# Optimization experiments

Measured on AMD Instinct MI355X. Metric: run time of the kernel, lower is better.

The kernel has to match this reference:

```python
import jax, jax.numpy as jnp
import numpy as np

NUM_NODES = 20000
NUM_EDGES = 65536
WIDTH = 64
EDGE_FEAT = 6
HIDDEN = 128


def setup_inputs() -> dict:
    key = jax.random.key(0)
    ks = jax.random.split(key, 6)
    x = jax.random.normal(ks[0], (NUM_NODES, WIDTH), dtype=jnp.float32)
    edge_attr = jax.random.normal(ks[1], (NUM_EDGES, EDGE_FEAT), dtype=jnp.float32)
    # weight-generating MLP params (the `nn` callable), fan-in scaled
    W1 = jax.random.normal(ks[2], (EDGE_FEAT, HIDDEN), dtype=jnp.float32) / np.sqrt(EDGE_FEAT)
    b1 = jnp.zeros((HIDDEN,), dtype=jnp.float32)
    W2 = jax.random.normal(ks[3], (HIDDEN, WIDTH * WIDTH), dtype=jnp.float32) / np.sqrt(HIDDEN)
    b2 = jnp.zeros((WIDTH * WIDTH,), dtype=jnp.float32)
    senders = jax.random.randint(ks[4], (NUM_EDGES,), 0, NUM_NODES)
    receivers = jax.random.randint(ks[5], (NUM_EDGES,), 0, NUM_NODES)
    return {"x": x, "edge_attr": edge_attr, "W1": W1, "b1": b1,
            "W2": W2, "b2": b2, "senders": senders, "receivers": receivers}


def reference(x, edge_attr, W1, b1, W2, b2, senders, receivers):
    n_segs, width = x.shape
    # nn(edge_attr): (E, width*width) edge-conditioned weights
    h = jax.nn.relu(edge_attr @ W1 + b1)
    weight = (h @ W2 + b2).reshape(-1, width, width)  # (E, w, w)
    # gather sender features, per-edge (1,w) @ (w,w) matmul -> (E, w)
    msgs = jnp.einsum('ew,ewv->ev', x[senders], weight)
    # scatter-sum messages into receiver nodes (aggr == 'sum')
    return jax.ops.segment_sum(msgs, receivers, num_segments=n_segs)
```

## Files before the change

kernel.cpp:

```cpp
#include <hip/hip_runtime.h>
#include <stdint.h>

typedef _Float16 f16;
typedef f16 f16x8 __attribute__((ext_vector_type(8)));
typedef float f32x4 __attribute__((ext_vector_type(4)));

#define NUM_NODES 20000
#define NUM_EDGES 65536
#define WIDTH 64
#define EDGE_FEAT 6
#define HIDDEN 128
#define BM 64
#define PADCH 132
#define XPAD 72

#define XH_HALFS (NUM_NODES * WIDTH)
#define XCONV_BLKS 625
#define W2G_HALFS (PADCH * 4096)
#define OUT_FLOATS (NUM_NODES * WIDTH)
#define ZBLKS 313

__device__ __forceinline__ void gload_lds16(const f16* g, f16* l) {
  __builtin_amdgcn_global_load_lds(
      (const __attribute__((address_space(1))) unsigned int*)g,
      (__attribute__((address_space(3))) unsigned int*)l, 16, 0, 0);
}

__global__ __launch_bounds__(256) void prep_kernel(
    const float* __restrict__ x, const float* __restrict__ W2,
    const float* __restrict__ b2, f16* __restrict__ ws_h,
    float* __restrict__ out)
{
  f16* x_h = ws_h;
  f16* W2g = ws_h + XH_HALFS;
  const int blk = blockIdx.x, tid = threadIdx.x;

  if (blk < PADCH) {
    const int ki = blk;
    if (ki > HIDDEN) {
      f16x8 z;
      #pragma unroll
      for (int u = 0; u < 8; ++u) z[u] = (f16)0.f;
      *(f16x8*)&W2g[(size_t)ki * 4096 + tid * 16] = z;
      *(f16x8*)&W2g[(size_t)ki * 4096 + tid * 16 + 8] = z;
      return;
    }
    __shared__ float row[4096];
    const float* srcrow;
    if (ki < HIDDEN) {
      const float4* src = (const float4*)(W2 + (size_t)ki * 4096);
      #pragma unroll
      for (int i = 0; i < 4; ++i) {
        float4 v = src[tid + 256 * i];
        *(float4*)&row[(tid + 256 * i) * 4] = v;
      }
      __syncthreads();
      srcrow = row;
    } else {
      srcrow = b2;
    }
    const int obase = tid * 16;
    f16x8 outv0, outv1;
    #pragma unroll
    for (int u = 0; u < 8; ++u) {
      int o = obase + u;
      int n = o >> 6, pg = (o >> 3) & 7, j = o & 7;
      int k = (pg ^ (n & 7)) * 8 + j;
      outv0[u] = (f16)srcrow[k * 64 + n];
    }
    #pragma unroll
    for (int u = 0; u < 8; ++u) {
      int o = obase + 8 + u;
      int n = o >> 6, pg = (o >> 3) & 7, j = o & 7;
      int k = (pg ^ (n & 7)) * 8 + j;
      outv1[u] = (f16)srcrow[k * 64 + n];
    }
    *(f16x8*)&W2g[(size_t)ki * 4096 + obase] = outv0;
    *(f16x8*)&W2g[(size_t)ki * 4096 + obase + 8] = outv1;
  } else if (blk < PADCH + XCONV_BLKS) {
    int idx = (blk - PADCH) * 2048 + tid * 8;
    if (idx + 8 <= XH_HALFS) {
      float4 a = *(const float4*)(x + idx);
      float4 b = *(const float4*)(x + idx + 4);
      f16x8 hv;
      hv[0] = (f16)a.x; hv[1] = (f16)a.y; hv[2] = (f16)a.z; hv[3] = (f16)a.w;
      hv[4] = (f16)b.x; hv[5] = (f16)b.y; hv[6] = (f16)b.z; hv[7] = (f16)b.w;
      *(f16x8*)&x_h[idx] = hv;
    }
  } else {
    int base = (blk - PADCH - XCONV_BLKS) * 4096 + tid * 16;
    float4 z = {0.f, 0.f, 0.f, 0.f};
    #pragma unroll
    for (int i = 0; i < 4; ++i) {
      int idx = base + i * 4;
      if (idx + 4 <= OUT_FLOATS) *(float4*)(out + idx) = z;
    }
  }
}

__global__ __launch_bounds__(256, 4) void nnconv_kernel(
    const float* __restrict__ ea, const float* __restrict__ W1,
    const float* __restrict__ b1, const int* __restrict__ senders,
    const int* __restrict__ receivers, const f16* __restrict__ ws_h,
    float* __restrict__ out)
{
  const f16* x_h = ws_h;
  const f16* W2g = ws_h + XH_HALFS;
  __shared__ __align__(16) f16 xt[BM][XPAD];
  __shared__ __align__(16) f16 Bb[2][4096];

  const int tid = threadIdx.x;
  const int lane = tid & 63, wid = tid >> 6;
  const int quad = lane >> 4, l15 = lane & 15;
  const int mhalf = wid >> 1, nhalf = wid & 1;
  const int e0 = blockIdx.x * BM;
  const int mbase = mhalf * 32;

#define STAGE(CI, SP)                                                         \
  {                                                                           \
    _Pragma("unroll") for (int i_ = 0; i_ < 2; ++i_) {                        \
      int slice_ = wid + 4 * i_;                                              \
      gload_lds16(W2g + (size_t)(CI) * 4096 + slice_ * 512 + (lane << 3),     \
                  &Bb[SP][slice_ * 512]);                                     \
    }                                                                         \
  }
  STAGE(0, 0);

  {
    int r = tid >> 2, q = tid & 3;
    int s = senders[e0 + r];
    const uint4* src = (const uint4*)(x_h + (size_t)s * WIDTH + q * 16);
    uint4* dst = (uint4*)&xt[r][q * 16];
    dst[0] = src[0];
    dst[1] = src[1];
  }

  float ear[2][6];
  #pragma unroll
  for (int t = 0; t < 2; ++t) {
    const float* p = ea + (size_t)(e0 + mbase + t * 16 + l15) * EDGE_FEAT;
    #pragma unroll
    for (int f = 0; f < 6; ++f) ear[t][f] = p[f];
  }

  int boff[2][2];
  #pragma unroll
  for (int kc = 0; kc < 2; ++kc)
    #pragma unroll
    for (int nt = 0; nt < 2; ++nt) {
      int n = nhalf * 32 + nt * 16 + l15;
      int g = kc * 4 + quad;
      boff[kc][nt] = n * 64 + (g ^ (n & 7)) * 8;
    }

#define HCOMP(KI, HV)                                                         \
  {                                                                           \
    float b1c_ = b1[(KI)];                                                    \
    float w1c_[6];                                                            \
    _Pragma("unroll") for (int f = 0; f < 6; ++f)                             \
      w1c_[f] = W1[f * HIDDEN + (KI)];                                        \
    _Pragma("unroll") for (int t = 0; t < 2; ++t) {                           \
      float s_ = b1c_;                                                        \
      _Pragma("unroll") for (int f = 0; f < 6; ++f)                           \
        s_ = fmaf(ear[t][f], w1c_[f], s_);                                    \
      HV[t] = (f16)fmaxf(s_, 0.f);                                            \
    }                                                                         \
  }

  f16 hnxt[2];
  HCOMP(0, hnxt);

  __syncthreads();

  f16x8 xf[2][2];
  #pragma unroll
  for (int t = 0; t < 2; ++t)
    #pragma unroll
    for (int kc = 0; kc < 2; ++kc)
      xf[t][kc] = *(const f16x8*)&xt[mbase + t * 16 + l15][kc * 32 + quad * 8];

  f32x4 acc[2][2];
  #pragma unroll
  for (int t = 0; t < 2; ++t)
    #pragma unroll
    for (int nt = 0; nt < 2; ++nt)
      acc[t][nt] = (f32x4){0.f, 0.f, 0.f, 0.f};

  #pragma unroll 1
  for (int k = 0; k < 128; ++k) {
    asm volatile("s_waitcnt vmcnt(0) lgkmcnt(0)\n\ts_barrier" ::: "memory");
    __builtin_amdgcn_sched_barrier(0);
    STAGE(k + 1, (k + 1) & 1);
    __builtin_amdgcn_sched_barrier(0);

    f16 hv[2];
    #pragma unroll
    for (int t = 0; t < 2; ++t) hv[t] = hnxt[t];

    const f16* gb = &Bb[k & 1][0];
    f16x8 bf[2][2];
    #pragma unroll
    for (int kc = 0; kc < 2; ++kc)
      #pragma unroll
      for (int nt = 0; nt < 2; ++nt)
        bf[kc][nt] = *(const f16x8*)&gb[boff[kc][nt]];

    int kn = (k + 1 < 128) ? k + 1 : 127;
    HCOMP(kn, hnxt);

    f16x8 sa0[2], sa1[2];
    #pragma unroll
    for (int t = 0; t < 2; ++t) {
      sa0[t] = xf[t][0] * hv[t];
      sa1[t] = xf[t][1] * hv[t];
    }
    __builtin_amdgcn_s_setprio(1);
    #pragma unroll
    for (int t = 0; t < 2; ++t)
      #pragma unroll
      for (int nt = 0; nt < 2; ++nt)
        acc[t][nt] = __builtin_amdgcn_mfma_f32_16x16x32_f16(
            sa0[t], bf[0][nt], acc[t][nt], 0, 0, 0);
    #pragma unroll
    for (int t = 0; t < 2; ++t)
      #pragma unroll
      for (int nt = 0; nt < 2; ++nt)
        acc[t][nt] = __builtin_amdgcn_mfma_f32_16x16x32_f16(
            sa1[t], bf[1][nt], acc[t][nt], 0, 0, 0);
    __builtin_amdgcn_s_setprio(0);
  }

  asm volatile("s_waitcnt vmcnt(0) lgkmcnt(0)\n\ts_barrier" ::: "memory");
  __builtin_amdgcn_sched_barrier(0);
  {
    f16x8 bf[2][2];
    #pragma unroll
    for (int kc = 0; kc < 2; ++kc)
      #pragma unroll
      for (int nt = 0; nt < 2; ++nt)
        bf[kc][nt] = *(const f16x8*)&Bb[0][boff[kc][nt]];
    __builtin_amdgcn_s_setprio(1);
    #pragma unroll
    for (int t = 0; t < 2; ++t)
      #pragma unroll
      for (int nt = 0; nt < 2; ++nt) {
        acc[t][nt] = __builtin_amdgcn_mfma_f32_16x16x32_f16(
            xf[t][0], bf[0][nt], acc[t][nt], 0, 0, 0);
        acc[t][nt] = __builtin_amdgcn_mfma_f32_16x16x32_f16(
            xf[t][1], bf[1][nt], acc[t][nt], 0, 0, 0);
      }
    __builtin_amdgcn_s_setprio(0);
  }
#undef STAGE
#undef HCOMP

  #pragma unroll
  for (int t = 0; t < 2; ++t) {
    int ebase = e0 + mbase + t * 16 + quad * 4;
    int rc[4];
    #pragma unroll
    for (int r = 0; r < 4; ++r) rc[r] = receivers[ebase + r];
    #pragma unroll
    for (int nt = 0; nt < 2; ++nt) {
      int v = nhalf * 32 + nt * 16 + l15;
      #pragma unroll
      for (int r = 0; r < 4; ++r)
        atomicAdd(out + (size_t)rc[r] * WIDTH + v, acc[t][nt][r]);
    }
  }
}

extern "C" void kernel_launch(void* const* d_in, const int* in_sizes, int n_in,
                              void* d_out, int out_size, void* d_ws, size_t ws_size,
                              hipStream_t stream) {
  const float* x  = (const float*)d_in[0];
  const float* ea = (const float*)d_in[1];
  const float* W1 = (const float*)d_in[2];
  const float* b1 = (const float*)d_in[3];
  const float* W2 = (const float*)d_in[4];
  const float* b2 = (const float*)d_in[5];
  const int* snd  = (const int*)d_in[6];
  const int* rcv  = (const int*)d_in[7];
  float* out = (float*)d_out;
  f16* wsh = (f16*)d_ws;

  const int prep_grid = PADCH + XCONV_BLKS + ZBLKS;
  prep_kernel<<<prep_grid, 256, 0, stream>>>(x, W2, b2, wsh, out);
  nnconv_kernel<<<NUM_EDGES / BM, 256, 0, stream>>>(ea, W1, b1, snd, rcv, wsh, out);
}
```

Measured before the change: 160.6 us.

## Precompute hidden activations in LDS and deepen W2 staging ring

Doubles the edge tile to 128 edges per 512-thread block. The ReLU hidden layer for all 128 edges is computed up front into an LDS buffer, replacing the per-iteration recomputation of the first MLP in the K loop. The double buffer for W2 chunks becomes a 4-slot ring prefetched three chunks ahead, with partial vmcnt waits instead of draining all loads each iteration, and the loop is unrolled by 4. The cost is much higher LDS use per block (about 80KB, with x tile padding removed), which limits blocks per CU and may add bank conflicts on the x tile.

```diff
diff --git a/kernel.cpp b/kernel.cpp
--- a/kernel.cpp
+++ b/kernel.cpp
@@ -10,13 +10,11 @@
 #define WIDTH 64
 #define EDGE_FEAT 6
 #define HIDDEN 128
-#define BM 64
+#define BM 128
 #define PADCH 132
-#define XPAD 72
 
 #define XH_HALFS (NUM_NODES * WIDTH)
 #define XCONV_BLKS 625
-#define W2G_HALFS (PADCH * 4096)
 #define OUT_FLOATS (NUM_NODES * WIDTH)
 #define ZBLKS 313
 
@@ -98,7 +96,7 @@
   }
 }
 
-__global__ __launch_bounds__(256, 4) void nnconv_kernel(
+__global__ __launch_bounds__(512, 4) void nnconv_kernel(
     const float* __restrict__ ea, const float* __restrict__ W1,
     const float* __restrict__ b1, const int* __restrict__ senders,
     const int* __restrict__ receivers, const f16* __restrict__ ws_h,
@@ -106,25 +104,45 @@
 {
   const f16* x_h = ws_h;
   const f16* W2g = ws_h + XH_HALFS;
-  __shared__ __align__(16) f16 xt[BM][XPAD];
-  __shared__ __align__(16) f16 Bb[2][4096];
+  __shared__ __align__(16) f16 xt[BM][64];
+  __shared__ __align__(16) f16 hbuf[HIDDEN * 128];
+  __shared__ __align__(16) f16 ring[4 * 4096];
 
   const int tid = threadIdx.x;
   const int lane = tid & 63, wid = tid >> 6;
   const int quad = lane >> 4, l15 = lane & 15;
-  const int mhalf = wid >> 1, nhalf = wid & 1;
+  const int mq = wid >> 1, nh = wid & 1;
   const int e0 = blockIdx.x * BM;
-  const int mbase = mhalf * 32;
-
-#define STAGE(CI, SP)                                                         \
-  {                                                                           \
-    _Pragma("unroll") for (int i_ = 0; i_ < 2; ++i_) {                        \
-      int slice_ = wid + 4 * i_;                                              \
-      gload_lds16(W2g + (size_t)(CI) * 4096 + slice_ * 512 + (lane << 3),     \
-                  &Bb[SP][slice_ * 512]);                                     \
-    }                                                                         \
-  }
-  STAGE(0, 0);
+  const int mbase = mq * 32;
+
+  float* eaf = (float*)&xt[0][0];
+  if (tid < 192)
+    ((float4*)eaf)[tid] = ((const float4*)(ea + (size_t)e0 * EDGE_FEAT))[tid];
+  __syncthreads();
+
+  {
+    const int k = tid >> 2, q4 = tid & 3;
+    float b1c = b1[k];
+    float w1c[6];
+    #pragma unroll
+    for (int f = 0; f < 6; ++f) w1c[f] = W1[f * HIDDEN + k];
+    f16* hrow = &hbuf[k * 128 + q4 * 32];
+    const float* er = eaf + q4 * 32 * EDGE_FEAT;
+    #pragma unroll
+    for (int g8 = 0; g8 < 4; ++g8) {
+      f16x8 hv;
+      #pragma unroll
+      for (int j = 0; j < 8; ++j) {
+        const float* p = er + (g8 * 8 + j) * EDGE_FEAT;
+        float s = b1c;
+        #pragma unroll
+        for (int f = 0; f < 6; ++f) s = fmaf(p[f], w1c[f], s);
+        hv[j] = (f16)fmaxf(s, 0.f);
+      }
+      *(f16x8*)&hrow[g8 * 8] = hv;
+    }
+  }
+  __syncthreads();
 
   {
     int r = tid >> 2, q = tid & 3;
@@ -134,50 +152,30 @@
     dst[0] = src[0];
     dst[1] = src[1];
   }
-
-  float ear[2][6];
-  #pragma unroll
-  for (int t = 0; t < 2; ++t) {
-    const float* p = ea + (size_t)(e0 + mbase + t * 16 + l15) * EDGE_FEAT;
-    #pragma unroll
-    for (int f = 0; f < 6; ++f) ear[t][f] = p[f];
-  }
+  const f16* wsl = W2g + wid * 512 + (lane << 3);
+  gload_lds16(wsl,            &ring[0 * 4096 + wid * 512]);
+  gload_lds16(wsl + 1 * 4096, &ring[1 * 4096 + wid * 512]);
+  gload_lds16(wsl + 2 * 4096, &ring[2 * 4096 + wid * 512]);
+  __syncthreads();
+
+  f16x8 xf[2][2];
+  #pragma unroll
+  for (int t = 0; t < 2; ++t)
+    #pragma unroll
+    for (int kc = 0; kc < 2; ++kc)
+      xf[t][kc] = *(const f16x8*)&xt[mbase + t * 16 + l15][kc * 32 + quad * 8];
 
   int boff[2][2];
   #pragma unroll
   for (int kc = 0; kc < 2; ++kc)
     #pragma unroll
     for (int nt = 0; nt < 2; ++nt) {
-      int n = nhalf * 32 + nt * 16 + l15;
+      int n = nh * 32 + nt * 16 + l15;
       int g = kc * 4 + quad;
       boff[kc][nt] = n * 64 + (g ^ (n & 7)) * 8;
     }
 
-#define HCOMP(KI, HV)                                                         \
-  {                                                                           \
-    float b1c_ = b1[(KI)];                                                    \
-    float w1c_[6];                                                            \
-    _Pragma("unroll") for (int f = 0; f < 6; ++f)                             \
-      w1c_[f] = W1[f * HIDDEN + (KI)];                                        \
-    _Pragma("unroll") for (int t = 0; t < 2; ++t) {                           \
-      float s_ = b1c_;                                                        \
-      _Pragma("unroll") for (int f = 0; f < 6; ++f)                           \
-        s_ = fmaf(ear[t][f], w1c_[f], s_);                                    \
-      HV[t] = (f16)fmaxf(s_, 0.f);                                            \
-    }                                                                         \
-  }
-
-  f16 hnxt[2];
-  HCOMP(0, hnxt);
-
-  __syncthreads();
-
-  f16x8 xf[2][2];
-  #pragma unroll
-  for (int t = 0; t < 2; ++t)
-    #pragma unroll
-    for (int kc = 0; kc < 2; ++kc)
-      xf[t][kc] = *(const f16x8*)&xt[mbase + t * 16 + l15][kc * 32 + quad * 8];
+  const f16* hb = &hbuf[mbase + l15];
 
   f32x4 acc[2][2];
   #pragma unroll
@@ -186,27 +184,25 @@
     for (int nt = 0; nt < 2; ++nt)
       acc[t][nt] = (f32x4){0.f, 0.f, 0.f, 0.f};
 
-  #pragma unroll 1
+  #pragma unroll 4
   for (int k = 0; k < 128; ++k) {
-    asm volatile("s_waitcnt vmcnt(0) lgkmcnt(0)\n\ts_barrier" ::: "memory");
+    asm volatile("s_waitcnt vmcnt(2)" ::: "memory");
+    __builtin_amdgcn_s_barrier();
     __builtin_amdgcn_sched_barrier(0);
-    STAGE(k + 1, (k + 1) & 1);
+    gload_lds16(wsl + (size_t)(k + 3) * 4096,
+                &ring[((k + 3) & 3) * 4096 + wid * 512]);
     __builtin_amdgcn_sched_barrier(0);
 
+    const f16* gb = &ring[(k & 3) * 4096];
+    f16x8 bf[2][2];
+    #pragma unroll
+    for (int kc = 0; kc < 2; ++kc)
+      #pragma unroll
+      for (int nt = 0; nt < 2; ++nt)
+        bf[kc][nt] = *(const f16x8*)&gb[boff[kc][nt]];
     f16 hv[2];
     #pragma unroll
-    for (int t = 0; t < 2; ++t) hv[t] = hnxt[t];
-
-    const f16* gb = &Bb[k & 1][0];
-    f16x8 bf[2][2];
-    #pragma unroll
-    for (int kc = 0; kc < 2; ++kc)
-      #pragma unroll
-      for (int nt = 0; nt < 2; ++nt)
-        bf[kc][nt] = *(const f16x8*)&gb[boff[kc][nt]];
-
-    int kn = (k + 1 < 128) ? k + 1 : 127;
-    HCOMP(kn, hnxt);
+    for (int t = 0; t < 2; ++t) hv[t] = hb[k * 128 + t * 16];
 
     f16x8 sa0[2], sa1[2];
     #pragma unroll
@@ -230,7 +226,8 @@
     __builtin_amdgcn_s_setprio(0);
   }
 
-  asm volatile("s_waitcnt vmcnt(0) lgkmcnt(0)\n\ts_barrier" ::: "memory");
+  asm volatile("s_waitcnt vmcnt(2)" ::: "memory");
+  __builtin_amdgcn_s_barrier();
   __builtin_amdgcn_sched_barrier(0);
   {
     f16x8 bf[2][2];
@@ -238,7 +235,7 @@
     for (int kc = 0; kc < 2; ++kc)
       #pragma unroll
       for (int nt = 0; nt < 2; ++nt)
-        bf[kc][nt] = *(const f16x8*)&Bb[0][boff[kc][nt]];
+        bf[kc][nt] = *(const f16x8*)&ring[boff[kc][nt]];
     __builtin_amdgcn_s_setprio(1);
     #pragma unroll
     for (int t = 0; t < 2; ++t)
@@ -251,8 +248,6 @@
       }
     __builtin_amdgcn_s_setprio(0);
   }
-#undef STAGE
-#undef HCOMP
 
   #pragma unroll
   for (int t = 0; t < 2; ++t) {
@@ -262,7 +257,7 @@
     for (int r = 0; r < 4; ++r) rc[r] = receivers[ebase + r];
     #pragma unroll
     for (int nt = 0; nt < 2; ++nt) {
-      int v = nhalf * 32 + nt * 16 + l15;
+      int v = nh * 32 + nt * 16 + l15;
       #pragma unroll
       for (int r = 0; r < 4; ++r)
         atomicAdd(out + (size_t)rc[r] * WIDTH + v, acc[t][nt][r]);
@@ -286,5 +281,5 @@
 
   const int prep_grid = PADCH + XCONV_BLKS + ZBLKS;
   prep_kernel<<<prep_grid, 256, 0, stream>>>(x, W2, b2, wsh, out);
-  nnconv_kernel<<<NUM_EDGES / BM, 256, 0, stream>>>(ea, W1, b1, snd, rcv, wsh, out);
-}
+  nnconv_kernel<<<NUM_EDGES / BM, 512, 0, stream>>>(ea, W1, b1, snd, rcv, wsh, out);
+}
```

After: 147.9 us. 1.09x faster.
